# Kernel optimization log

Hardware: AMD Instinct MI355X
Metric: run time of the kernel (lower is better)

The kernel has to match this reference:

```python
import jax, jax.numpy as jnp
import numpy as np


def setup_inputs() -> dict:
    key = jax.random.key(0)
    k1, k2, k3 = jax.random.split(key, 3)
    B, S, DB, DW, W = 64, 512, 768, 100, 512
    bert_x = jax.random.normal(k1, (B, S, DB), dtype=jnp.float32)
    w2v_input = jax.random.normal(k2, (B, W, DW), dtype=jnp.float32)
    mappings = jax.random.randint(k3, (B, S - 1), 0, W, dtype=jnp.int32)
    return {"bert_x": bert_x, "w2v_input": w2v_input, "mappings": mappings}


def reference(bert_x, w2v_input, mappings):
    # bert_x: [B, S, DB] (frozen SciBERT last_hidden_state)
    # w2v_input: [B, W, DW] (FastText word vectors)
    # mappings: [B, S-1] int; loop breaks at first -1, writes row i+1
    B, S, DB = bert_x.shape
    DW = w2v_input.shape[2]
    dt = bert_x.dtype
    # loop-break semantics: valid only while all previous mappings != -1
    valid = jnp.cumprod((mappings != -1).astype(jnp.int32), axis=1).astype(dt)  # [B, S-1]
    safe = jnp.clip(mappings, 0)
    w2v_g = jnp.take_along_axis(w2v_input, safe[..., None], axis=1)  # [B, S-1, DW]
    body = jnp.concatenate(
        [bert_x[:, 1:, :] * valid[..., None], w2v_g * valid[..., None]], axis=-1
    )  # [B, S-1, DB+DW]
    zero_row = jnp.zeros((B, 1, DB + DW), dtype=dt)  # CLS row stays zero
    return jnp.concatenate([zero_row, body], axis=1)  # [B, S, DB+DW]
```

## Files before the change

### kernel.cpp

```cpp
#include <hip/hip_runtime.h>
#include <hip/hip_bf16.h>


#define B_    64
#define S_    512
#define SM1_  511
#define DB_   768
#define DW_   100
#define DOUT_ 868
#define DOUT4_ 217
#define DB4_  192
#define DW4_  25
#define W_    512
#define BLKS_PER_BATCH_ 31
#define K_    14

typedef float fvec4 __attribute__((ext_vector_type(4)));

__global__ __launch_bounds__(256) void fused_flat_kernel(
        const float* __restrict__ bert_x,
        const float* __restrict__ w2v,
        const int* __restrict__ mappings,
        float* __restrict__ out) {
    const int blk   = blockIdx.x;
    const int b     = blk / BLKS_PER_BATCH_;
    const int chunk = blk - b * BLKS_PER_BATCH_;
    const int tid   = threadIdx.x;

    __shared__ int s_min;
    if (tid == 0) s_min = SM1_;
    __syncthreads();
    const int* __restrict__ mrow = mappings + b * SM1_;
    for (int i = tid; i < SM1_; i += 256) {
        if (mrow[i] == -1) atomicMin(&s_min, i);
    }
    __syncthreads();
    const int fi = s_min;

    const fvec4* __restrict__ bbase = reinterpret_cast<const fvec4*>(
        bert_x + (size_t)b * S_ * DB_);
    const fvec4* __restrict__ wbase = reinterpret_cast<const fvec4*>(
        w2v + (size_t)b * W_ * DW_);
    fvec4* __restrict__ obase = reinterpret_cast<fvec4*>(
        out + (size_t)b * S_ * DOUT_);

    const int idx0 = chunk * (256 * K_) + tid;

    fvec4 v[K_];
    #pragma unroll
    for (int k = 0; k < K_; ++k) {
        const int idx = idx0 + k * 256;
        const int row = idx / DOUT4_;
        const int c4  = idx - row * DOUT4_;
        fvec4 val = (fvec4)(0.f);
        const bool valid = (row != 0) && ((row - 1) < fi);
        if (valid) {
            if (c4 < DB4_) {
                val = bbase[(size_t)row * DB4_ + c4];
            } else {
                int w = mrow[row - 1];
                if (w < 0) w = 0;
                val = wbase[(size_t)w * DW4_ + (c4 - DB4_)];
            }
        }
        v[k] = val;
    }

    #pragma unroll
    for (int k = 0; k < K_; ++k) {
        __builtin_nontemporal_store(v[k], &obase[idx0 + k * 256]);
    }
}

extern "C" void kernel_launch(void* const* d_in, const int* in_sizes, int n_in,
                              void* d_out, int out_size, void* d_ws, size_t ws_size,
                              hipStream_t stream) {
    const float* bert_x = (const float*)d_in[0];
    const float* w2v    = (const float*)d_in[1];
    const int* mappings = (const int*)d_in[2];
    float* out = (float*)d_out;

    fused_flat_kernel<<<B_ * BLKS_PER_BATCH_, 256, 0, stream>>>(
        bert_x, w2v, mappings, out);
}
```

Measured before the change: 40.01 us.

## Speculatively load rows before computing -1 cutoff via wave shuffle reduction

Replaces the shared-memory atomicMin scan and its two block barriers with a per-wave register scan of the mappings row followed by a shuffle min-reduction. The bert and w2v loads are now issued speculatively before the cutoff is known, and masking happens at store time, so the scan overlaps with the main memory traffic. It also halves the per-thread work (K 14 to 7, doubling the number of blocks) and adds an occupancy hint to launch bounds. The cost is that every wave re-reads the full mappings row, and rows past the cutoff are read even though they are later zeroed.

```diff
diff --git a/kernel.cpp b/kernel.cpp
--- a/kernel.cpp
+++ b/kernel.cpp
@@ -12,12 +12,12 @@
 #define DB4_  192
 #define DW4_  25
 #define W_    512
-#define BLKS_PER_BATCH_ 31
-#define K_    14
+#define K_    7
+#define BLKS_PER_BATCH_ 62
 
 typedef float fvec4 __attribute__((ext_vector_type(4)));
 
-__global__ __launch_bounds__(256) void fused_flat_kernel(
+__global__ __launch_bounds__(256, 8) void fused_spec_kernel(
         const float* __restrict__ bert_x,
         const float* __restrict__ w2v,
         const int* __restrict__ mappings,
@@ -26,16 +26,16 @@
     const int b     = blk / BLKS_PER_BATCH_;
     const int chunk = blk - b * BLKS_PER_BATCH_;
     const int tid   = threadIdx.x;
+    const int lane  = tid & 63;
 
-    __shared__ int s_min;
-    if (tid == 0) s_min = SM1_;
-    __syncthreads();
     const int* __restrict__ mrow = mappings + b * SM1_;
-    for (int i = tid; i < SM1_; i += 256) {
-        if (mrow[i] == -1) atomicMin(&s_min, i);
+
+    int sm[8];
+    #pragma unroll
+    for (int j = 0; j < 8; ++j) {
+        const int i = lane + j * 64;
+        sm[j] = (i < SM1_) ? mrow[i] : 0;
     }
-    __syncthreads();
-    const int fi = s_min;
 
     const fvec4* __restrict__ bbase = reinterpret_cast<const fvec4*>(
         bert_x + (size_t)b * S_ * DB_);
@@ -52,23 +52,35 @@
         const int idx = idx0 + k * 256;
         const int row = idx / DOUT4_;
         const int c4  = idx - row * DOUT4_;
-        fvec4 val = (fvec4)(0.f);
-        const bool valid = (row != 0) && ((row - 1) < fi);
-        if (valid) {
-            if (c4 < DB4_) {
-                val = bbase[(size_t)row * DB4_ + c4];
-            } else {
-                int w = mrow[row - 1];
-                if (w < 0) w = 0;
-                val = wbase[(size_t)w * DW4_ + (c4 - DB4_)];
-            }
+        if (c4 < DB4_) {
+            v[k] = bbase[(size_t)row * DB4_ + c4];
+        } else {
+            const int wr = (row > 0) ? (row - 1) : 0;
+            int w = mrow[wr];
+            if (w < 0) w = 0;
+            v[k] = wbase[(size_t)w * DW4_ + (c4 - DB4_)];
         }
-        v[k] = val;
+    }
+
+    int m = SM1_;
+    #pragma unroll
+    for (int j = 0; j < 8; ++j) {
+        const int i = lane + j * 64;
+        if (sm[j] == -1 && i < m) m = i;
+    }
+    #pragma unroll
+    for (int off = 32; off > 0; off >>= 1) {
+        const int o = __shfl_xor(m, off, 64);
+        if (o < m) m = o;
     }
 
     #pragma unroll
     for (int k = 0; k < K_; ++k) {
-        __builtin_nontemporal_store(v[k], &obase[idx0 + k * 256]);
+        const int idx = idx0 + k * 256;
+        const int row = idx / DOUT4_;
+        const bool valid = (row != 0) && ((row - 1) < m);
+        fvec4 o = valid ? v[k] : (fvec4)(0.f);
+        __builtin_nontemporal_store(o, &obase[idx]);
     }
 }
 
@@ -80,6 +92,6 @@
     const int* mappings = (const int*)d_in[2];
     float* out = (float*)d_out;
 
-    fused_flat_kernel<<<B_ * BLKS_PER_BATCH_, 256, 0, stream>>>(
+    fused_spec_kernel<<<B_ * BLKS_PER_BATCH_, 256, 0, stream>>>(
         bert_x, w2v, mappings, out);
 }
```

Measured after the change: 39.54 us. Within noise of the previous version (-1.2%).
